# Kernel tuning notes

Measured on AMD Instinct MI355X. Metric: run time of the kernel, lower is better.

Reference implementation:

```python
import jax, jax.numpy as jnp
import numpy as np

B, S, D = 4, 2048, 1024  # batch, seq_len, input_dimension
KD, VD = 1024, 1024      # key_dim, value_dim


def setup_inputs() -> dict:
    key = jax.random.key(0)
    ks = jax.random.split(key, 9)
    sc_in = 1.0 / np.sqrt(D)
    sc_v = 1.0 / np.sqrt(VD)
    return {
        "x":  jax.random.normal(ks[0], (B, S, D), dtype=jnp.float32),
        "Wq": jax.random.normal(ks[1], (KD, D), dtype=jnp.float32) * sc_in,
        "bq": jax.random.normal(ks[2], (KD,), dtype=jnp.float32) * 0.01,
        "Wk": jax.random.normal(ks[3], (KD, D), dtype=jnp.float32) * sc_in,
        "bk": jax.random.normal(ks[4], (KD,), dtype=jnp.float32) * 0.01,
        "Wv": jax.random.normal(ks[5], (VD, D), dtype=jnp.float32) * sc_in,
        "bv": jax.random.normal(ks[6], (VD,), dtype=jnp.float32) * 0.01,
        "Wo": jax.random.normal(ks[7], (D, VD), dtype=jnp.float32) * sc_v,
        "bo": jax.random.normal(ks[8], (D,), dtype=jnp.float32) * 0.01,
    }


def reference(x, Wq, bq, Wk, bk, Wv, bv, Wo, bo):
    # projections (torch Linear: x @ W.T + b)
    q = jnp.einsum('bsd,kd->bsk', x, Wq) + bq   # (B,S,KD)
    k = jnp.einsum('bsd,kd->bsk', x, Wk) + bk   # (B,S,KD)
    v = jnp.einsum('bsd,vd->bsv', x, Wv) + bv   # (B,S,VD)

    scores = jnp.einsum('bqk,bsk->bqs', q, k) / jnp.sqrt(jnp.float32(KD))  # (B,S,S)

    # sign rescale: scores * sign(scores) (sign(0) mapped to 1) == |scores| with zeros kept
    sign_mask = jnp.sign(scores)
    sign_mask = sign_mask + (sign_mask == 0).astype(jnp.float32)

    # causal mask: lower-triangular (incl diag) multiplied by 1, strict upper -> -inf
    seq = scores.shape[-1]
    causal = jnp.tril(jnp.ones((seq, seq), dtype=bool))
    masked = jnp.where(causal, scores * sign_mask, -jnp.inf)

    weights = jax.nn.softmax(masked, axis=2)            # (B,S,S)
    out = jnp.einsum('bqs,bsv->bqv', weights, v)        # (B,S,VD)
    return jnp.einsum('bqv,dv->bqd', out, Wo) + bo      # (B,S,D)
```

## Files before the change

### kernel.cpp

```cpp
#include <hip/hip_runtime.h>
#include <hip/hip_bf16.h>
#include <cstdint>


#define BM 128

typedef __attribute__((ext_vector_type(8))) __bf16 bf16x8;
typedef __attribute__((ext_vector_type(4))) __bf16 bf16x4;
typedef __attribute__((ext_vector_type(4))) float floatx4;

struct Ptr3 { const float* p[3]; };

__device__ __forceinline__ void async_copy16(const __bf16* g, const __bf16* l) {
  __builtin_amdgcn_global_load_lds(
      (const __attribute__((address_space(1))) unsigned int*)(const void*)g,
      (__attribute__((address_space(3))) unsigned int*)(unsigned)(uintptr_t)(const void*)l,
      16, 0, 0);
}

__device__ __forceinline__ void gemm_core(const __bf16* __restrict__ pA,
                                          const __bf16* __restrict__ pB,
                                          int K, int kBeg, int kEnd, int mb,
                                          int nb, floatx4 (&acc)[4][4]) {
  __shared__ __align__(16) __bf16 As0[BM * 32];
  __shared__ __align__(16) __bf16 As1[BM * 32];
  __shared__ __align__(16) __bf16 Bs0[BM * 32];
  __shared__ __align__(16) __bf16 Bs1[BM * 32];

  const int t = threadIdx.x;
  const int lane = t & 63;
  const int wave = t >> 6;
  const int quad = lane >> 4;
  const int l16 = lane & 15;
  const int wm = wave >> 1;
  const int wn = wave & 1;

  const __bf16* gA = pA + (long)(mb * BM + (t >> 2)) * K + ((t & 3) * 8);
  const __bf16* gB = pB + (long)(nb * BM + (t >> 2)) * K + ((t & 3) * 8);
  const long rowHalf = (long)64 * K;
  __bf16* lA0 = &As0[t * 8];
  __bf16* lA1 = &As1[t * 8];
  __bf16* lB0 = &Bs0[t * 8];
  __bf16* lB1 = &Bs1[t * 8];

  for (int kk = kBeg; kk < kEnd; ++kk) {
    const long ko = (long)kk * 64;
    async_copy16(gA + ko, lA0);
    async_copy16(gA + ko + rowHalf, lA0 + 2048);
    async_copy16(gA + ko + 32, lA1);
    async_copy16(gA + ko + 32 + rowHalf, lA1 + 2048);
    async_copy16(gB + ko, lB0);
    async_copy16(gB + ko + rowHalf, lB0 + 2048);
    async_copy16(gB + ko + 32, lB1);
    async_copy16(gB + ko + 32 + rowHalf, lB1 + 2048);
    __syncthreads();

#pragma unroll
    for (int p = 0; p < 2; ++p) {
      const __bf16* As = p ? As1 : As0;
      const __bf16* Bs = p ? Bs1 : Bs0;
      bf16x8 af[4], bfr[4];
#pragma unroll
      for (int i = 0; i < 4; ++i) {
        af[i] = *(const bf16x8*)&As[(wm * 64 + i * 16 + l16) * 32 + quad * 8];
        bfr[i] = *(const bf16x8*)&Bs[(wn * 64 + i * 16 + l16) * 32 + quad * 8];
      }
#pragma unroll
      for (int i = 0; i < 4; ++i)
#pragma unroll
        for (int j = 0; j < 4; ++j)
          acc[i][j] = __builtin_amdgcn_mfma_f32_16x16x32_bf16(af[i], bfr[j],
                                                              acc[i][j], 0, 0, 0);
    }
    __syncthreads();
  }
}

__global__ void __launch_bounds__(256, 2)
fusedA(const __bf16* __restrict__ xb, const __bf16* __restrict__ Wb,
       const float* __restrict__ bq, const float* __restrict__ bk,
       __bf16* __restrict__ qk, const __bf16* __restrict__ Wob,
       const __bf16* __restrict__ Wvt, __bf16* __restrict__ Wvo,
       int S, int KD, int B) {
  const int id = blockIdx.x;
  const __bf16 *pA, *pB;
  int mb, nb, z;
  if (id < 1024) {
    const int xcd = id & 7;
    const int j = id >> 3;
    mb = xcd * 8 + (j & 7);
    const int rest = j >> 3;
    nb = rest & 7;
    z = rest >> 3;
    pA = xb;
    pB = Wb + ((long)z << 20);
  } else {
    const int wid = id - 1024;
    mb = wid >> 3;
    nb = wid & 7;
    z = 2;
    pA = Wob;
    pB = Wvt;
  }

  floatx4 acc[4][4] = {};
  gemm_core(pA, pB, KD, 0, KD / 64, mb, nb, acc);

  const int t = threadIdx.x;
  const int lane = t & 63, wave = t >> 6;
  const int rb = (wave >> 1) * 64 + (lane >> 4) * 4;
  const int cb = (wave & 1) * 64 + (lane & 15);

  if (z < 2) {
    __bf16* C = qk + (long)z * B * S * KD;
    const float* bz = z ? bk : bq;
#pragma unroll
    for (int j4 = 0; j4 < 4; ++j4) {
      const int gc = nb * 128 + cb + j4 * 16;
      const float bv = bz[gc];
#pragma unroll
      for (int i = 0; i < 4; ++i) {
        const int gr = mb * BM + rb + i * 16;
#pragma unroll
        for (int r = 0; r < 4; ++r)
          C[(long)(gr + r) * KD + gc] = (__bf16)(acc[i][j4][r] + bv);
      }
    }
  } else {
#pragma unroll
    for (int j4 = 0; j4 < 4; ++j4) {
      const int gc = nb * 128 + cb + j4 * 16;
#pragma unroll
      for (int i = 0; i < 4; ++i) {
        const int gr = mb * BM + rb + i * 16;
#pragma unroll
        for (int r = 0; r < 4; ++r)
          Wvo[(long)(gr + r) * 1024 + gc] = (__bf16)acc[i][j4][r];
      }
    }
  }
}

__global__ void __launch_bounds__(256, 2)
fusedB(const __bf16* __restrict__ xb, const __bf16* __restrict__ Wvo,
       const float* __restrict__ bvo, __bf16* __restrict__ Ut,
       const __bf16* __restrict__ q, const __bf16* __restrict__ k,
       __bf16* __restrict__ P, float* __restrict__ lsum,
       int S, int KD, int D) {
  const int id = blockIdx.x;
  const __bf16 *pA, *pB;
  int mb, nb, b, mode;
  if (id < 512) {
    const int xcd = id & 7;
    const int j = id >> 3;
    mb = xcd * 8 + (j & 7);
    nb = j >> 3;
    b = 0;
    mode = 0;
    pA = xb;
    pB = Wvo;
  } else {
    const int sid = id - 512;
    const int xcd = sid & 7;
    const int r = sid >> 3;
    b = r / 17;
    const int ci = r - b * 17;
    const int n1 = xcd + 1;
    mb = (ci < n1) ? xcd : (15 - xcd);
    nb = (ci < n1) ? ci : (ci - n1);
    mode = 1;
    pA = q + (long)b * S * KD;
    pB = k + (long)b * S * KD;
  }

  floatx4 acc[4][4] = {};
  gemm_core(pA, pB, KD, 0, KD / 64, mb, nb, acc);

  const int t = threadIdx.x;
  const int lane = t & 63, wave = t >> 6;
  const int l16 = lane & 15;
  const int rb = (wave >> 1) * 64 + (lane >> 4) * 4;
  const int cb = (wave & 1) * 64 + l16;

  if (mode == 0) {
    const int bb = (mb * BM) / S;
    const int s0 = mb * BM - bb * S;
#pragma unroll
    for (int j4 = 0; j4 < 4; ++j4) {
      const int gc = nb * 128 + cb + j4 * 16;
      const float bv = bvo[gc];
#pragma unroll
      for (int i = 0; i < 4; ++i) {
        const int sr = s0 + rb + i * 16;
        bf16x4 o;
#pragma unroll
        for (int r = 0; r < 4; ++r) o[r] = (__bf16)(acc[i][j4][r] + bv);
        *(bf16x4*)&Ut[((long)bb * D + gc) * S + sr] = o;
      }
    }
  } else {
    __bf16* C = P + (long)b * S * S;
    float* lrow = lsum + (long)b * S;
    const float sc = 0.03125f;
#pragma unroll
    for (int i = 0; i < 4; ++i) {
#pragma unroll
      for (int r = 0; r < 4; ++r) {
        const int row = mb * BM + rb + i * 16 + r;
        float psum = 0.f;
#pragma unroll
        for (int j4 = 0; j4 < 4; ++j4) {
          const int col = nb * 128 + cb + j4 * 16;
          const float p = (col <= row) ? __expf(fabsf(acc[i][j4][r] * sc)) : 0.f;
          psum += p;
          C[(long)row * S + col] = (__bf16)p;
        }
        psum += __shfl_xor(psum, 1, 64);
        psum += __shfl_xor(psum, 2, 64);
        psum += __shfl_xor(psum, 4, 64);
        psum += __shfl_xor(psum, 8, 64);
        if (l16 == 0) atomicAdd(&lrow[row], psum);
      }
    }
  }
}

__global__ void __launch_bounds__(256, 2)
gemm_pvo(const __bf16* __restrict__ P, const __bf16* __restrict__ Ut,
         const float* __restrict__ lsum, const float* __restrict__ bo,
         float* __restrict__ out, int S, int D) {
  const int id = blockIdx.x;
  const int xcd = id & 7;
  const int j = id >> 3;
  const int half = j >> 5;
  const int idx = j & 31;
  const int b = idx >> 3;
  const int nb = idx & 7;
  const int mb = half ? xcd : (15 - xcd);

  floatx4 acc[4][4] = {};
  gemm_core(P + (long)b * S * S, Ut + (long)b * D * S, S, 0, 2 * (mb + 1), mb,
            nb, acc);

  const int t = threadIdx.x;
  const int lane = t & 63, wave = t >> 6;
  const int rb = (wave >> 1) * 64 + (lane >> 4) * 4;
  const int cb = (wave & 1) * 64 + (lane & 15);
  const float* lrow = lsum + (long)b * S;

#pragma unroll
  for (int i = 0; i < 4; ++i) {
#pragma unroll
    for (int r = 0; r < 4; ++r) {
      const int row = mb * BM + rb + i * 16 + r;
      const float inv = 1.f / lrow[row];
#pragma unroll
      for (int j4 = 0; j4 < 4; ++j4) {
        const int col = nb * 128 + cb + j4 * 16;
        out[((long)b * S + row) * D + col] = acc[i][j4][r] * inv + bo[col];
      }
    }
  }
}

__global__ void prep(const float* __restrict__ x, Ptr3 wp,
                     const float* __restrict__ Wv, const float* __restrict__ bv,
                     __bf16* __restrict__ xb, __bf16* __restrict__ Wb,
                     __bf16* __restrict__ Wvt, float* __restrict__ bvo,
                     float* __restrict__ lsum) {
  __shared__ __bf16 tile[64][66];
  __shared__ float wsum[4];
  const int bid = blockIdx.x;
  const int t = threadIdx.x;
  if (bid < 8192) {
    const long i = ((long)bid * 256 + t) * 4;
    const float4 f = *(const float4*)(x + i);
    bf16x4 o;
    o[0] = (__bf16)f.x; o[1] = (__bf16)f.y; o[2] = (__bf16)f.z; o[3] = (__bf16)f.w;
    *(bf16x4*)(xb + i) = o;
  } else if (bid < 11264) {
    const int slot = (bid - 8192) * 256 + t;
    const int which = slot >> 18;
    const long e = (long)(slot & 0x3ffff) * 4;
    const float4 f = *(const float4*)(wp.p[which] + e);
    bf16x4 o;
    o[0] = (__bf16)f.x; o[1] = (__bf16)f.y; o[2] = (__bf16)f.z; o[3] = (__bf16)f.w;
    *(bf16x4*)(Wb + ((long)which << 20) + e) = o;
  } else if (bid < 11520) {
    const int idx = bid - 11264;
    const int r0 = (idx >> 4) * 64, c0 = (idx & 15) * 64;
#pragma unroll
    for (int e = 0; e < 16; ++e) {
      const int i = e * 256 + t;
      const int r = i >> 6, c = i & 63;
      tile[r][c] = (__bf16)Wv[(long)(r0 + r) * 1024 + (c0 + c)];
    }
    __syncthreads();
#pragma unroll
    for (int e = 0; e < 16; ++e) {
      const int i = e * 256 + t;
      const int r = i >> 6, c = i & 63;
      Wvt[(long)(c0 + r) * 1024 + (r0 + c)] = tile[c][r];
    }
  } else if (bid < 12544) {
    const int d = bid - 11520;
    const float* row = wp.p[2] + (long)d * 1024;
    float s = 0.f;
    for (int v = t; v < 1024; v += 256) s += bv[v] * row[v];
#pragma unroll
    for (int off = 32; off > 0; off >>= 1) s += __shfl_down(s, off, 64);
    if ((t & 63) == 0) wsum[t >> 6] = s;
    __syncthreads();
    if (t == 0) bvo[d] = wsum[0] + wsum[1] + wsum[2] + wsum[3];
  } else {
#pragma unroll
    for (int e = 0; e < 8; ++e)
      *(float4*)(lsum + (e * 256 + t) * 4) = float4{0.f, 0.f, 0.f, 0.f};
  }
}

extern "C" void kernel_launch(void* const* d_in, const int* in_sizes, int n_in,
                              void* d_out, int out_size, void* d_ws, size_t ws_size,
                              hipStream_t stream) {
  const float* x = (const float*)d_in[0];
  const float* Wq = (const float*)d_in[1];
  const float* bq = (const float*)d_in[2];
  const float* Wk = (const float*)d_in[3];
  const float* bk = (const float*)d_in[4];
  const float* Wv = (const float*)d_in[5];
  const float* bv = (const float*)d_in[6];
  const float* Wo = (const float*)d_in[7];
  const float* bo = (const float*)d_in[8];
  float* out = (float*)d_out;

  constexpr int B = 4, S = 2048, D = 1024, KD = 1024;
  constexpr long MB_ = 1024 * 1024;

  char* w = (char*)d_ws;
  __bf16* xb = (__bf16*)(w);
  __bf16* qk = (__bf16*)(w + 16 * MB_);
  __bf16* Ut = (__bf16*)(w + 48 * MB_);
  __bf16* P  = (__bf16*)(w + 64 * MB_);
  __bf16* Wb = (__bf16*)(w + 96 * MB_);
  __bf16* Wvt = (__bf16*)(w + 102 * MB_);
  __bf16* Wvo = (__bf16*)(w + 104 * MB_);
  float* lsum = (float*)(w + 106 * MB_);
  float* bvo = (float*)(w + 106 * MB_ + 65536);

  __bf16* Wob = Wb + (2l << 20);

  Ptr3 wp{{Wq, Wk, Wo}};
  prep<<<12545, 256, 0, stream>>>(x, wp, Wv, bv, xb, Wb, Wvt, bvo, lsum);

  fusedA<<<1088, 256, 0, stream>>>(xb, Wb, bq, bk, qk, Wob, Wvt, Wvo, S, KD, B);

  fusedB<<<1056, 256, 0, stream>>>(xb, Wvo, bvo, Ut, qk, qk + (long)B * S * KD,
                                   P, lsum, S, KD, D);

  gemm_pvo<<<512, 256, 0, stream>>>(P, Ut, lsum, bo, out, S, D);
}
```

Measured before the change: 248.6 us.

## Fold Wq and Wk into a combined matrix to replace separate Q/K projections

```diff
diff --git a/kernel.cpp b/kernel.cpp
--- a/kernel.cpp
+++ b/kernel.cpp
@@ -8,8 +8,6 @@
 typedef __attribute__((ext_vector_type(8))) __bf16 bf16x8;
 typedef __attribute__((ext_vector_type(4))) __bf16 bf16x4;
 typedef __attribute__((ext_vector_type(4))) float floatx4;
-
-struct Ptr3 { const float* p[3]; };
 
 __device__ __forceinline__ void async_copy16(const __bf16* g, const __bf16* l) {
   __builtin_amdgcn_global_load_lds(
@@ -76,151 +74,203 @@
   }
 }
 
+__device__ __forceinline__ float wave_sum(float s) {
+  s += __shfl_xor(s, 1, 64);
+  s += __shfl_xor(s, 2, 64);
+  s += __shfl_xor(s, 4, 64);
+  s += __shfl_xor(s, 8, 64);
+  s += __shfl_xor(s, 16, 64);
+  s += __shfl_xor(s, 32, 64);
+  return s;
+}
+
 __global__ void __launch_bounds__(256, 2)
-fusedA(const __bf16* __restrict__ xb, const __bf16* __restrict__ Wb,
-       const float* __restrict__ bq, const float* __restrict__ bk,
-       __bf16* __restrict__ qk, const __bf16* __restrict__ Wob,
-       const __bf16* __restrict__ Wvt, __bf16* __restrict__ Wvo,
-       int S, int KD, int B) {
+wcomb(const __bf16* __restrict__ Wqt, const __bf16* __restrict__ Wkt,
+      const __bf16* __restrict__ Wob, const __bf16* __restrict__ Wvt,
+      __bf16* __restrict__ Mqk, __bf16* __restrict__ Wvo,
+      const float* __restrict__ bq, const float* __restrict__ bk,
+      float* __restrict__ w1, float* __restrict__ w2, float* __restrict__ cbuf) {
   const int id = blockIdx.x;
-  const __bf16 *pA, *pB;
-  int mb, nb, z;
-  if (id < 1024) {
-    const int xcd = id & 7;
-    const int j = id >> 3;
-    mb = xcd * 8 + (j & 7);
-    const int rest = j >> 3;
-    nb = rest & 7;
-    z = rest >> 3;
-    pA = xb;
-    pB = Wb + ((long)z << 20);
-  } else {
-    const int wid = id - 1024;
-    mb = wid >> 3;
-    nb = wid & 7;
-    z = 2;
-    pA = Wob;
-    pB = Wvt;
-  }
-
-  floatx4 acc[4][4] = {};
-  gemm_core(pA, pB, KD, 0, KD / 64, mb, nb, acc);
-
-  const int t = threadIdx.x;
-  const int lane = t & 63, wave = t >> 6;
-  const int rb = (wave >> 1) * 64 + (lane >> 4) * 4;
-  const int cb = (wave & 1) * 64 + (lane & 15);
-
-  if (z < 2) {
-    __bf16* C = qk + (long)z * B * S * KD;
-    const float* bz = z ? bk : bq;
+  const int t = threadIdx.x;
+
+  if (id < 128) {
+    const bool isM = id < 64;
+    const int wid = isM ? id : (id - 64);
+    const int mb = wid >> 3, nb = wid & 7;
+    const __bf16* pA = isM ? Wkt : Wob;
+    const __bf16* pB = isM ? Wqt : Wvt;
+    __bf16* C = isM ? Mqk : Wvo;
+
+    floatx4 acc[4][4] = {};
+    gemm_core(pA, pB, 1024, 0, 16, mb, nb, acc);
+
+    const int lane = t & 63, wave = t >> 6;
+    const int rb = (wave >> 1) * 64 + (lane >> 4) * 4;
+    const int cb = (wave & 1) * 64 + (lane & 15);
 #pragma unroll
     for (int j4 = 0; j4 < 4; ++j4) {
       const int gc = nb * 128 + cb + j4 * 16;
-      const float bv = bz[gc];
 #pragma unroll
       for (int i = 0; i < 4; ++i) {
         const int gr = mb * BM + rb + i * 16;
 #pragma unroll
         for (int r = 0; r < 4; ++r)
-          C[(long)(gr + r) * KD + gc] = (__bf16)(acc[i][j4][r] + bv);
-      }
+          C[(long)(gr + r) * 1024 + gc] = (__bf16)acc[i][j4][r];
+      }
+    }
+  } else if (id < 144) {
+    const bool is1 = id < 136;
+    const int jb = is1 ? (id - 128) : (id - 136);
+    const __bf16* Wt = is1 ? Wqt : Wkt;
+    const float* bb = is1 ? bk : bq;
+    float* ow = is1 ? w1 : w2;
+    const int lane = t & 63, wave = t >> 6;
+    for (int rr = 0; rr < 32; ++rr) {
+      const int row = jb * 128 + wave * 32 + rr;
+      const bf16x8 a0 = *(const bf16x8*)&Wt[(long)row * 1024 + lane * 16];
+      const bf16x8 a1 = *(const bf16x8*)&Wt[(long)row * 1024 + lane * 16 + 8];
+      float s = 0.f;
+#pragma unroll
+      for (int e = 0; e < 8; ++e) {
+        s += (float)a0[e] * bb[lane * 16 + e];
+        s += (float)a1[e] * bb[lane * 16 + 8 + e];
+      }
+      s = wave_sum(s);
+      if (lane == 0) ow[row] = s;
     }
   } else {
-#pragma unroll
-    for (int j4 = 0; j4 < 4; ++j4) {
-      const int gc = nb * 128 + cb + j4 * 16;
-#pragma unroll
-      for (int i = 0; i < 4; ++i) {
-        const int gr = mb * BM + rb + i * 16;
-#pragma unroll
-        for (int r = 0; r < 4; ++r)
-          Wvo[(long)(gr + r) * 1024 + gc] = (__bf16)acc[i][j4][r];
-      }
-    }
+    __shared__ float wsum[4];
+    float s = 0.f;
+    for (int i = t; i < 1024; i += 256) s += bq[i] * bk[i];
+    s = wave_sum(s);
+    if ((t & 63) == 0) wsum[t >> 6] = s;
+    __syncthreads();
+    if (t == 0) cbuf[0] = wsum[0] + wsum[1] + wsum[2] + wsum[3];
   }
 }
 
 __global__ void __launch_bounds__(256, 2)
-fusedB(const __bf16* __restrict__ xb, const __bf16* __restrict__ Wvo,
-       const float* __restrict__ bvo, __bf16* __restrict__ Ut,
-       const __bf16* __restrict__ q, const __bf16* __restrict__ k,
-       __bf16* __restrict__ P, float* __restrict__ lsum,
-       int S, int KD, int D) {
+proj(const __bf16* __restrict__ xb, const __bf16* __restrict__ Mqk,
+     const __bf16* __restrict__ Wvo, const float* __restrict__ w2,
+     const float* __restrict__ bvo, const float* __restrict__ w1,
+     const float* __restrict__ cbuf, __bf16* __restrict__ yb,
+     __bf16* __restrict__ Ut, float* __restrict__ r1, int S, int D) {
   const int id = blockIdx.x;
-  const __bf16 *pA, *pB;
-  int mb, nb, b, mode;
-  if (id < 512) {
-    const int xcd = id & 7;
-    const int j = id >> 3;
-    mb = xcd * 8 + (j & 7);
-    nb = j >> 3;
-    b = 0;
-    mode = 0;
-    pA = xb;
-    pB = Wvo;
+  const int t = threadIdx.x;
+
+  if (id < 1024) {
+    const bool isY = id < 512;
+    const int pid = isY ? id : (id - 512);
+    const int xcd = pid & 7;
+    const int j = pid >> 3;
+    const int mb = xcd * 8 + (j & 7);
+    const int nb = j >> 3;
+    const __bf16* pB = isY ? Mqk : Wvo;
+
+    floatx4 acc[4][4] = {};
+    gemm_core(xb, pB, D, 0, D / 64, mb, nb, acc);
+
+    const int lane = t & 63, wave = t >> 6;
+    const int rb = (wave >> 1) * 64 + (lane >> 4) * 4;
+    const int cb = (wave & 1) * 64 + (lane & 15);
+
+    if (isY) {
+#pragma unroll
+      for (int j4 = 0; j4 < 4; ++j4) {
+        const int gc = nb * 128 + cb + j4 * 16;
+        const float bv = w2[gc];
+#pragma unroll
+        for (int i = 0; i < 4; ++i) {
+          const int gr = mb * BM + rb + i * 16;
+#pragma unroll
+          for (int r = 0; r < 4; ++r)
+            yb[(long)(gr + r) * D + gc] = (__bf16)(acc[i][j4][r] + bv);
+        }
+      }
+    } else {
+      const int bb = (mb * BM) / S;
+      const int s0 = mb * BM - bb * S;
+#pragma unroll
+      for (int j4 = 0; j4 < 4; ++j4) {
+        const int gc = nb * 128 + cb + j4 * 16;
+        const float bv = bvo[gc];
+#pragma unroll
+        for (int i = 0; i < 4; ++i) {
+          const int sr = s0 + rb + i * 16;
+          bf16x4 o;
+#pragma unroll
+          for (int r = 0; r < 4; ++r) o[r] = (__bf16)(acc[i][j4][r] + bv);
+          *(bf16x4*)&Ut[((long)bb * D + gc) * S + sr] = o;
+        }
+      }
+    }
   } else {
-    const int sid = id - 512;
-    const int xcd = sid & 7;
-    const int r = sid >> 3;
-    b = r / 17;
-    const int ci = r - b * 17;
-    const int n1 = xcd + 1;
-    mb = (ci < n1) ? xcd : (15 - xcd);
-    nb = (ci < n1) ? ci : (ci - n1);
-    mode = 1;
-    pA = q + (long)b * S * KD;
-    pB = k + (long)b * S * KD;
-  }
+    const int jb = id - 1024;
+    const float c = cbuf[0];
+    const int lane = t & 63, wave = t >> 6;
+    for (int rr = 0; rr < 32; ++rr) {
+      const int row = jb * 128 + wave * 32 + rr;
+      const bf16x8 a0 = *(const bf16x8*)&xb[(long)row * D + lane * 16];
+      const bf16x8 a1 = *(const bf16x8*)&xb[(long)row * D + lane * 16 + 8];
+      float s = 0.f;
+#pragma unroll
+      for (int e = 0; e < 8; ++e) {
+        s += (float)a0[e] * w1[lane * 16 + e];
+        s += (float)a1[e] * w1[lane * 16 + 8 + e];
+      }
+      s = wave_sum(s);
+      if (lane == 0) r1[row] = s + c;
+    }
+  }
+}
+
+__global__ void __launch_bounds__(256, 2)
+gemm_scores(const __bf16* __restrict__ yb, const __bf16* __restrict__ xb,
+            const float* __restrict__ r1, __bf16* __restrict__ P,
+            float* __restrict__ lsum, int S, int D) {
+  const int id = blockIdx.x;
+  const int xcd = id & 7;
+  const int r = id >> 3;
+  const int b = r / 17;
+  const int ci = r - b * 17;
+  const int n1 = xcd + 1;
+  const int mb = (ci < n1) ? xcd : (15 - xcd);
+  const int nb = (ci < n1) ? ci : (ci - n1);
 
   floatx4 acc[4][4] = {};
-  gemm_core(pA, pB, KD, 0, KD / 64, mb, nb, acc);
+  gemm_core(yb + (long)b * S * D, xb + (long)b * S * D, D, 0, D / 64, mb, nb,
+            acc);
 
   const int t = threadIdx.x;
   const int lane = t & 63, wave = t >> 6;
   const int l16 = lane & 15;
   const int rb = (wave >> 1) * 64 + (lane >> 4) * 4;
   const int cb = (wave & 1) * 64 + l16;
-
-  if (mode == 0) {
-    const int bb = (mb * BM) / S;
-    const int s0 = mb * BM - bb * S;
-#pragma unroll
-    for (int j4 = 0; j4 < 4; ++j4) {
-      const int gc = nb * 128 + cb + j4 * 16;
-      const float bv = bvo[gc];
-#pragma unroll
-      for (int i = 0; i < 4; ++i) {
-        const int sr = s0 + rb + i * 16;
-        bf16x4 o;
-#pragma unroll
-        for (int r = 0; r < 4; ++r) o[r] = (__bf16)(acc[i][j4][r] + bv);
-        *(bf16x4*)&Ut[((long)bb * D + gc) * S + sr] = o;
-      }
-    }
-  } else {
-    __bf16* C = P + (long)b * S * S;
-    float* lrow = lsum + (long)b * S;
-    const float sc = 0.03125f;
-#pragma unroll
-    for (int i = 0; i < 4; ++i) {
-#pragma unroll
-      for (int r = 0; r < 4; ++r) {
-        const int row = mb * BM + rb + i * 16 + r;
-        float psum = 0.f;
-#pragma unroll
-        for (int j4 = 0; j4 < 4; ++j4) {
-          const int col = nb * 128 + cb + j4 * 16;
-          const float p = (col <= row) ? __expf(fabsf(acc[i][j4][r] * sc)) : 0.f;
-          psum += p;
-          C[(long)row * S + col] = (__bf16)p;
-        }
-        psum += __shfl_xor(psum, 1, 64);
-        psum += __shfl_xor(psum, 2, 64);
-        psum += __shfl_xor(psum, 4, 64);
-        psum += __shfl_xor(psum, 8, 64);
-        if (l16 == 0) atomicAdd(&lrow[row], psum);
-      }
+  __bf16* C = P + (long)b * S * S;
+  float* lrow = lsum + (long)b * S;
+  const float* r1b = r1 + (long)b * S;
+  const float sc = 0.03125f;
+
+#pragma unroll
+  for (int i = 0; i < 4; ++i) {
+#pragma unroll
+    for (int r_ = 0; r_ < 4; ++r_) {
+      const int row = mb * BM + rb + i * 16 + r_;
+      const float rv = r1b[row];
+      float psum = 0.f;
+#pragma unroll
+      for (int j4 = 0; j4 < 4; ++j4) {
+        const int col = nb * 128 + cb + j4 * 16;
+        const float p =
+            (col <= row) ? __expf(fabsf((acc[i][j4][r_] + rv) * sc)) : 0.f;
+        psum += p;
+        C[(long)row * S + col] = (__bf16)p;
+      }
+      psum += __shfl_xor(psum, 1, 64);
+      psum += __shfl_xor(psum, 2, 64);
+      psum += __shfl_xor(psum, 4, 64);
+      psum += __shfl_xor(psum, 8, 64);
+      if (l16 == 0) atomicAdd(&lrow[row], psum);
     }
   }
 }
@@ -251,22 +301,24 @@
 #pragma unroll
   for (int i = 0; i < 4; ++i) {
 #pragma unroll
-    for (int r = 0; r < 4; ++r) {
-      const int row = mb * BM + rb + i * 16 + r;
+    for (int r_ = 0; r_ < 4; ++r_) {
+      const int row = mb * BM + rb + i * 16 + r_;
       const float inv = 1.f / lrow[row];
 #pragma unroll
       for (int j4 = 0; j4 < 4; ++j4) {
         const int col = nb * 128 + cb + j4 * 16;
-        out[((long)b * S + row) * D + col] = acc[i][j4][r] * inv + bo[col];
-      }
-    }
-  }
-}
-
-__global__ void prep(const float* __restrict__ x, Ptr3 wp,
-                     const float* __restrict__ Wv, const float* __restrict__ bv,
-                     __bf16* __restrict__ xb, __bf16* __restrict__ Wb,
-                     __bf16* __restrict__ Wvt, float* __restrict__ bvo,
+        out[((long)b * S + row) * D + col] = acc[i][j4][r_] * inv + bo[col];
+      }
+    }
+  }
+}
+
+__global__ void prep(const float* __restrict__ x, const float* __restrict__ Wq,
+                     const float* __restrict__ Wk, const float* __restrict__ Wv,
+                     const float* __restrict__ Wo, const float* __restrict__ bv,
+                     __bf16* __restrict__ xb, __bf16* __restrict__ Wqt,
+                     __bf16* __restrict__ Wkt, __bf16* __restrict__ Wvt,
+                     __bf16* __restrict__ Wob, float* __restrict__ bvo,
                      float* __restrict__ lsum) {
   __shared__ __bf16 tile[64][66];
   __shared__ float wsum[4];
@@ -278,33 +330,34 @@
     bf16x4 o;
     o[0] = (__bf16)f.x; o[1] = (__bf16)f.y; o[2] = (__bf16)f.z; o[3] = (__bf16)f.w;
     *(bf16x4*)(xb + i) = o;
-  } else if (bid < 11264) {
-    const int slot = (bid - 8192) * 256 + t;
-    const int which = slot >> 18;
-    const long e = (long)(slot & 0x3ffff) * 4;
-    const float4 f = *(const float4*)(wp.p[which] + e);
-    bf16x4 o;
-    o[0] = (__bf16)f.x; o[1] = (__bf16)f.y; o[2] = (__bf16)f.z; o[3] = (__bf16)f.w;
-    *(bf16x4*)(Wb + ((long)which << 20) + e) = o;
-  } else if (bid < 11520) {
-    const int idx = bid - 11264;
+  } else if (bid < 8960) {
+    const int which = (bid - 8192) >> 8;
+    const int idx = (bid - 8192) & 255;
+    const float* src = which == 0 ? Wq : (which == 1 ? Wk : Wv);
+    __bf16* dst = which == 0 ? Wqt : (which == 1 ? Wkt : Wvt);
     const int r0 = (idx >> 4) * 64, c0 = (idx & 15) * 64;
 #pragma unroll
     for (int e = 0; e < 16; ++e) {
       const int i = e * 256 + t;
       const int r = i >> 6, c = i & 63;
-      tile[r][c] = (__bf16)Wv[(long)(r0 + r) * 1024 + (c0 + c)];
+      tile[r][c] = (__bf16)src[(long)(r0 + r) * 1024 + (c0 + c)];
     }
     __syncthreads();
 #pragma unroll
     for (int e = 0; e < 16; ++e) {
       const int i = e * 256 + t;
       const int r = i >> 6, c = i & 63;
-      Wvt[(long)(c0 + r) * 1024 + (r0 + c)] = tile[c][r];
-    }
-  } else if (bid < 12544) {
-    const int d = bid - 11520;
-    const float* row = wp.p[2] + (long)d * 1024;
+      dst[(long)(c0 + r) * 1024 + (r0 + c)] = tile[c][r];
+    }
+  } else if (bid < 9984) {
+    const long i = ((long)(bid - 8960) * 256 + t) * 4;
+    const float4 f = *(const float4*)(Wo + i);
+    bf16x4 o;
+    o[0] = (__bf16)f.x; o[1] = (__bf16)f.y; o[2] = (__bf16)f.z; o[3] = (__bf16)f.w;
+    *(bf16x4*)(Wob + i) = o;
+  } else if (bid < 11008) {
+    const int d = bid - 9984;
+    const float* row = Wo + (long)d * 1024;
     float s = 0.f;
     for (int v = t; v < 1024; v += 256) s += bv[v] * row[v];
 #pragma unroll
@@ -333,29 +386,37 @@
   const float* bo = (const float*)d_in[8];
   float* out = (float*)d_out;
 
-  constexpr int B = 4, S = 2048, D = 1024, KD = 1024;
+  constexpr int B = 4, S = 2048, D = 1024;
   constexpr long MB_ = 1024 * 1024;
 
   char* w = (char*)d_ws;
-  __bf16* xb = (__bf16*)(w);
-  __bf16* qk = (__bf16*)(w + 16 * MB_);
-  __bf16* Ut = (__bf16*)(w + 48 * MB_);
-  __bf16* P  = (__bf16*)(w + 64 * MB_);
-  __bf16* Wb = (__bf16*)(w + 96 * MB_);
-  __bf16* Wvt = (__bf16*)(w + 102 * MB_);
-  __bf16* Wvo = (__bf16*)(w + 104 * MB_);
-  float* lsum = (float*)(w + 106 * MB_);
-  float* bvo = (float*)(w + 106 * MB_ + 65536);
-
-  __bf16* Wob = Wb + (2l << 20);
-
-  Ptr3 wp{{Wq, Wk, Wo}};
-  prep<<<12545, 256, 0, stream>>>(x, wp, Wv, bv, xb, Wb, Wvt, bvo, lsum);
-
-  fusedA<<<1088, 256, 0, stream>>>(xb, Wb, bq, bk, qk, Wob, Wvt, Wvo, S, KD, B);
-
-  fusedB<<<1056, 256, 0, stream>>>(xb, Wvo, bvo, Ut, qk, qk + (long)B * S * KD,
-                                   P, lsum, S, KD, D);
+  __bf16* xb  = (__bf16*)(w);
+  __bf16* yb  = (__bf16*)(w + 16 * MB_);
+  __bf16* Ut  = (__bf16*)(w + 32 * MB_);
+  __bf16* P   = (__bf16*)(w + 48 * MB_);
+  __bf16* Mqk = (__bf16*)(w + 80 * MB_);
+  __bf16* Wvo = (__bf16*)(w + 82 * MB_);
+  __bf16* Wqt = (__bf16*)(w + 84 * MB_);
+  __bf16* Wkt = (__bf16*)(w + 86 * MB_);
+  __bf16* Wvt = (__bf16*)(w + 88 * MB_);
+  __bf16* Wob = (__bf16*)(w + 90 * MB_);
+  float* lsum = (float*)(w + 92 * MB_);
+  float* r1   = (float*)(w + 92 * MB_ + 32768);
+  float* w1   = (float*)(w + 92 * MB_ + 65536);
+  float* w2   = (float*)(w + 92 * MB_ + 69632);
+  float* bvo  = (float*)(w + 92 * MB_ + 73728);
+  float* cbuf = (float*)(w + 92 * MB_ + 77824);
+
+  prep<<<11009, 256, 0, stream>>>(x, Wq, Wk, Wv, Wo, bv, xb, Wqt, Wkt, Wvt,
+                                  Wob, bvo, lsum);
+
+  wcomb<<<145, 256, 0, stream>>>(Wqt, Wkt, Wob, Wvt, Mqk, Wvo, bq, bk, w1, w2,
+                                 cbuf);
+
+  proj<<<1088, 256, 0, stream>>>(xb, Mqk, Wvo, w2, bvo, w1, cbuf, yb, Ut, r1,
+                                 S, D);
+
+  gemm_scores<<<544, 256, 0, stream>>>(yb, xb, r1, P, lsum, S, D);
 
   gemm_pvo<<<512, 256, 0, stream>>>(P, Ut, lsum, bo, out, S, D);
 }
```

Measured after the change: 253.5 us. Within noise of the previous version (+2.0%).
